# Performance work log

Hardware: AMD Instinct MI355X
Metric: run time of the kernel (lower is better)

## Reference

```python
import jax, jax.numpy as jnp
import numpy as np

B, T, Fd, C, D = 16, 256, 128, 32, 32
K_RATIO = 0.5
EPS = 1e-5


def setup_inputs() -> dict:
    key = jax.random.key(0)
    ks = jax.random.split(key, 40)
    n = lambda i, shape, s=0.05: jax.random.normal(ks[i], shape, jnp.float32) * s
    inp = {"x": jax.random.normal(ks[0], (B, T, Fd, C), jnp.float32)}
    inp.update(c1w=n(1, (C, C)), c1b=n(2, (C,)), bng=1.0 + n(3, (C,)), bnb=n(4, (C,)),
               bnm=n(5, (C,)), bnv=jax.random.uniform(ks[6], (C,)) + 0.5,
               c2w=n(7, (1, C)), c2b=n(8, (1,)))
    def gat_params(i0, pre):
        return {pre + "apw": n(i0, (D, C)), pre + "apb": n(i0 + 1, (D,)),
                pre + "aw": n(i0 + 2, (D,)), pre + "pww": n(i0 + 3, (D, C)),
                pre + "pwb": n(i0 + 4, (D,)), pre + "pow": n(i0 + 5, (D, C)),
                pre + "pob": n(i0 + 6, (D,)), pre + "g": 1.0 + n(i0 + 7, (D,)),
                pre + "be": n(i0 + 8, (D,)), pre + "m": n(i0 + 9, (D,)),
                pre + "v": jax.random.uniform(ks[i0 + 10], (D,)) + 0.5}
    inp.update(gat_params(9, "fc_"))
    inp.update(gat_params(20, "tc_"))
    inp.update(pfw=n(31, (1, D)), pfb=n(32, (1,)), ptw=n(33, (1, D)), ptb=n(34, (1,)),
               w1=n(35, (D, D)), w2=n(36, (D, D)), fcw=n(37, (2, 2 * D)), fcb=n(38, (2,)))
    return inp


def _gat(h, apw, apb, aw, pww, pwb, poww, pob, g, be, mu, var):
    # h: (B, N, C). Dense pairwise multiplication -> (B, N, N, C)
    p = h[:, :, None, :] * h[:, None, :, :]
    e = jnp.tanh(jnp.einsum('bijc,dc->bijd', p, apw) + apb)      # (B,N,N,D)
    att = jax.nn.softmax(jnp.einsum('bijd,d->bij', e, aw), axis=2)  # softmax over dim=-2 (temp=1)
    out = jnp.einsum('bij,bjc->bic', att, h) @ pww.T + pwb + h @ poww.T + pob
    out = (out - mu) / jnp.sqrt(var + EPS) * g + be               # BatchNorm1d (eval)
    return jax.nn.selu(out)


def _pool(h, pw, pb, ratio):
    s = jax.nn.sigmoid(h @ pw.T + pb)                # (B,N,1)
    kn = max(int(h.shape[1] * ratio), 1)
    _, idx = jax.lax.top_k(s[..., 0], kn)            # (B,kn), descending scores
    return jnp.take_along_axis(h * s, idx[..., None], axis=1)


def reference(x, c1w, c1b, bng, bnb, bnm, bnv, c2w, c2b,
              fc_apw, fc_apb, fc_aw, fc_pww, fc_pwb, fc_pow, fc_pob, fc_g, fc_be, fc_m, fc_v,
              tc_apw, tc_apb, tc_aw, tc_pww, tc_pwb, tc_pow, tc_pob, tc_g, tc_be, tc_m, tc_v,
              pfw, pfb, ptw, ptb, w1, w2, fcw, fcb):
    # conv1 (1x1), SELU, BatchNorm2d (eval), conv2 (1x1 -> 1 channel)
    xp = jnp.einsum('oc,btfc->botf', c1w, x) + c1b[None, :, None, None]
    xp = jax.nn.selu(xp)
    xp = (xp - bnm[None, :, None, None]) / jnp.sqrt(bnv + EPS)[None, :, None, None] \
         * bng[None, :, None, None] + bnb[None, :, None, None]
    m = jnp.einsum('c,bctf->btf', c2w[0], xp) + c2b[0]           # (B,T,F)
    M0 = jax.nn.softmax(m, axis=1)
    FCatt = jnp.einsum('btf,btfc->bfc', M0, x)                   # sum over T
    TCatt = jnp.einsum('btf,btfc->btc', M0, x)                   # sum over F
    FC_gat = _gat(FCatt, fc_apw, fc_apb, fc_aw, fc_pww, fc_pwb, fc_pow, fc_pob, fc_g, fc_be, fc_m, fc_v)
    TC_gat = _gat(TCatt, tc_apw, tc_apb, tc_aw, tc_pww, tc_pwb, tc_pow, tc_pob, tc_g, tc_be, tc_m, tc_v)
    xF = _pool(FC_gat, pfw, pfb, K_RATIO)                        # (B, F/2, D)
    xT = _pool(TC_gat, ptw, ptb, K_RATIO)                        # (B, T/2, D)
    M1 = jax.nn.softmax((xF @ w1.T) @ xT.transpose(0, 2, 1), axis=-1)
    M2 = jax.nn.softmax((xT @ w2.T) @ xF.transpose(0, 2, 1), axis=-1)
    xF_fused = xF + M1 @ xT
    xT_fused = xT + M2 @ xF
    node = jnp.concatenate([xF_fused.max(axis=1), xT_fused.max(axis=1)], axis=-1)
    return node @ fcw.T + fcb
```

## Files before the change

kernel.cpp:

```cpp
#include <hip/hip_runtime.h>
#include <hip/hip_bf16.h>

#define Bn 16
#define Tn 256
#define Fn 128
#define Cn 32
#define Dn 32
#define EPSf 1e-5f
#define SELU_L 1.0507009873554805f
#define SELU_A 1.6732632423543772f

typedef unsigned short u16;
typedef unsigned int u32;

struct Ptrs { const void* p[39]; };

#define P_C1W 0
#define P_C1B 1024
#define P_MW  1056
#define P_MK  1088
#define P_FC  1089
#define P_TCG (1089+3264)
#define G_APW 0
#define G_APB 1024
#define G_AW  1056
#define G_PWW 1088
#define G_PWB 2112
#define G_POW 2144
#define G_POB 3168
#define G_GS  3200
#define G_GB  3232
#define GAT_SZ 3264
#define P_PFW (P_TCG+GAT_SZ)
#define P_PFB (P_PFW+32)
#define P_PTW (P_PFB+1)
#define P_PTB (P_PTW+32)
#define P_W1  (P_PTB+1)
#define P_W2  (P_W1+1024)
#define P_FCW (P_W2+1024)
#define P_FCB (P_FCW+128)
#define P_FLAG 10000

#define WS_M     10240
#define WS_FCATT (WS_M+524288)
#define WS_TCATT (WS_FCATT+65536)
#define WS_FCGAT (WS_TCATT+131072)
#define WS_TCGAT (WS_FCGAT+65536)
#define WS_XF    (WS_TCGAT+131072)
#define WS_XT    (WS_XF+32768)
#define WS_XFF   (WS_XT+65536)
#define WS_XTF   (WS_XFF+32768)
#define WS_YFC   (WS_XTF+65536)
#define WS_ZFC   (WS_YFC+65536)
#define WS_YTC   (WS_ZFC+65536)
#define WS_ZTC   (WS_YTC+131072)
#define WS_SFC   (WS_ZTC+131072)

__device__ __forceinline__ float bf2f(u16 u) {
    union { u32 i; float f; } v; v.i = ((u32)u) << 16; return v.f;
}
__device__ __forceinline__ u16 f2bf(float f) {
    union { float f; u32 u; } v; v.f = f;
    u32 r = (v.u + 0x7fffu + ((v.u >> 16) & 1u)) >> 16;
    return (u16)r;
}
__device__ __forceinline__ void up2(u32 u, float* o) {
    union { u32 i; float f; } a, b;
    a.i = u << 16; b.i = u & 0xffff0000u;
    o[0] = a.f; o[1] = b.f;
}
__device__ __forceinline__ float tanh_fast(float x) {
    float e = __expf(2.f * x);
    return 1.f - 2.f / (e + 1.f);
}
__device__ __forceinline__ float ldp(const void* p, int i, int isb) {
    return isb ? bf2f(((const u16*)p)[i]) : ((const float*)p)[i];
}

__global__ void k0_setup(Ptrs in, float* __restrict__ P) {
    __shared__ int sflag;
    int tid = threadIdx.x;
    if (tid == 0) {
        const u16* xu = (const u16*)in.p[0];
        int bad = 0;
        for (int i = 0; i < 256; i++) {
            float f = bf2f(xu[i]);
            float a = fabsf(f);
            if (!(a < 64.f) && !(a == 0.f)) bad++;
        }
        sflag = (bad <= 8) ? 1 : 0;
        P[P_FLAG] = (float)sflag;
    }
    __syncthreads();
    const int isb = sflag;

    for (int i = tid; i < 1024; i += 256) P[P_C1W + i] = ldp(in.p[1], i, isb);
    if (tid < 32) {
        P[P_C1B + tid] = ldp(in.p[2], tid, isb);
        float A = ldp(in.p[3], tid, isb) * rsqrtf(ldp(in.p[6], tid, isb) + EPSf);
        P[P_MW + tid] = ldp(in.p[7], tid, isb) * A * SELU_L;
    }
    if (tid == 0) {
        float k = ldp(in.p[8], 0, isb);
        for (int o = 0; o < 32; o++) {
            float A = ldp(in.p[3], o, isb) * rsqrtf(ldp(in.p[6], o, isb) + EPSf);
            float Bc = ldp(in.p[4], o, isb) - ldp(in.p[5], o, isb) * A;
            k += ldp(in.p[7], o, isb) * Bc;
        }
        P[P_MK] = k;
    }
    for (int g = 0; g < 2; g++) {
        int ib = g ? 20 : 9;
        float* G = P + (g ? P_TCG : P_FC);
        for (int i = tid; i < 1024; i += 256) {
            G[G_APW + i] = ldp(in.p[ib + 0], i, isb);
            G[G_PWW + i] = ldp(in.p[ib + 3], i, isb);
            G[G_POW + i] = ldp(in.p[ib + 5], i, isb);
        }
        if (tid < 32) {
            G[G_APB + tid] = ldp(in.p[ib + 1], tid, isb);
            G[G_AW  + tid] = ldp(in.p[ib + 2], tid, isb);
            G[G_PWB + tid] = ldp(in.p[ib + 4], tid, isb);
            G[G_POB + tid] = ldp(in.p[ib + 6], tid, isb);
            float gs = ldp(in.p[ib + 7], tid, isb) * rsqrtf(ldp(in.p[ib + 10], tid, isb) + EPSf);
            G[G_GS + tid] = gs;
            G[G_GB + tid] = ldp(in.p[ib + 8], tid, isb) - ldp(in.p[ib + 9], tid, isb) * gs;
        }
    }
    if (tid < 32) {
        P[P_PFW + tid] = ldp(in.p[31], tid, isb);
        P[P_PTW + tid] = ldp(in.p[33], tid, isb);
    }
    if (tid == 0) { P[P_PFB] = ldp(in.p[32], 0, isb); P[P_PTB] = ldp(in.p[34], 0, isb); }
    for (int i = tid; i < 1024; i += 256) {
        P[P_W1 + i] = ldp(in.p[35], i, isb);
        P[P_W2 + i] = ldp(in.p[36], i, isb);
    }
    if (tid < 128) P[P_FCW + tid] = ldp(in.p[37], tid, isb);
    if (tid < 2)   P[P_FCB + tid] = ldp(in.p[38], tid, isb);
}

__global__ __launch_bounds__(256) void k1_conv_m(const void* __restrict__ xin,
                                                 const float* __restrict__ P,
                                                 float* __restrict__ M) {
    int idx = blockIdx.x * 256 + threadIdx.x;
    const int isb = __builtin_amdgcn_readfirstlane((int)P[P_FLAG]);
    float xv[32];
    if (isb) {
        const uint4* xp4 = reinterpret_cast<const uint4*>((const u16*)xin + (size_t)idx * 32);
        uint4 q0 = xp4[0], q1 = xp4[1], q2 = xp4[2], q3 = xp4[3];
        up2(q0.x, xv + 0);  up2(q0.y, xv + 2);  up2(q0.z, xv + 4);  up2(q0.w, xv + 6);
        up2(q1.x, xv + 8);  up2(q1.y, xv + 10); up2(q1.z, xv + 12); up2(q1.w, xv + 14);
        up2(q2.x, xv + 16); up2(q2.y, xv + 18); up2(q2.z, xv + 20); up2(q2.w, xv + 22);
        up2(q3.x, xv + 24); up2(q3.y, xv + 26); up2(q3.z, xv + 28); up2(q3.w, xv + 30);
    } else {
        const float4* xf4 = reinterpret_cast<const float4*>((const float*)xin + (size_t)idx * 32);
        #pragma unroll
        for (int q = 0; q < 8; q++) {
            float4 v = xf4[q];
            xv[q * 4 + 0] = v.x; xv[q * 4 + 1] = v.y;
            xv[q * 4 + 2] = v.z; xv[q * 4 + 3] = v.w;
        }
    }
    float acc = P[P_MK];
    #pragma unroll
    for (int o = 0; o < 32; o++) {
        float z = P[P_C1B + o];
        #pragma unroll
        for (int c = 0; c < 32; c++) z = fmaf(P[P_C1W + o * 32 + c], xv[c], z);
        float br = (z > 0.f) ? z : SELU_A * (__expf(z) - 1.f);
        acc = fmaf(P[P_MW + o], br, acc);
    }
    M[idx] = acc;
}

__global__ __launch_bounds__(256) void k2_softmax(float* __restrict__ M,
                                                  float* __restrict__ FCzero) {
    __shared__ float r[256];
    int b = blockIdx.x >> 3, fg = blockIdx.x & 7;
    int tid = threadIdx.x;
    int fl = tid & 15, ts = tid >> 4;
    float* col = M + (size_t)b * (Tn * Fn) + fg * 16 + fl;
    float v[16];
    float mx = -1e30f;
    #pragma unroll
    for (int k = 0; k < 16; k++) { v[k] = col[(ts * 16 + k) * Fn]; mx = fmaxf(mx, v[k]); }
    r[tid] = mx; __syncthreads();
    for (int s = 128; s >= 16; s >>= 1) { if (tid < s) r[tid] = fmaxf(r[tid], r[tid + s]); __syncthreads(); }
    mx = r[fl];
    __syncthreads();
    float sm = 0.f;
    #pragma unroll
    for (int k = 0; k < 16; k++) { v[k] = __expf(v[k] - mx); sm += v[k]; }
    r[tid] = sm; __syncthreads();
    for (int s = 128; s >= 16; s >>= 1) { if (tid < s) r[tid] += r[tid + s]; __syncthreads(); }
    float inv = 1.f / r[fl];
    #pragma unroll
    for (int k = 0; k < 16; k++) col[(ts * 16 + k) * Fn] = v[k] * inv;
    int gid = blockIdx.x * 256 + tid;
    for (int i = gid; i < Bn * Fn * Cn; i += 128 * 256) FCzero[i] = 0.f;
}

__global__ __launch_bounds__(256) void k3n(const void* __restrict__ xin,
                                           const float* __restrict__ M,
                                           const float* __restrict__ Pflag,
                                           float* __restrict__ FCatt,
                                           float* __restrict__ TCatt) {
    __shared__ float lA[256], lB[256];
    int bi = blockIdx.x;
    int b = bi >> 5, tg = bi & 31;
    int tid = threadIdx.x;
    const int isb = __builtin_amdgcn_readfirstlane((int)Pflag[P_FLAG]);
    float fa0[8], fa1[8];
    #pragma unroll
    for (int k = 0; k < 8; k++) { fa0[k] = 0.f; fa1[k] = 0.f; }
    int fbase = tid >> 4;
    for (int tt = 0; tt < 8; tt++) {
        int t = tg * 8 + tt;
        const float* Mrow = M + (size_t)b * (Tn * Fn) + (size_t)t * Fn;
        size_t rowoff = ((size_t)b * Tn + t) * (Fn * Cn);
        float ts0 = 0.f, ts1 = 0.f;
        #pragma unroll
        for (int k = 0; k < 8; k++) {
            float x0, x1;
            if (isb) {
                u32 u = *(const u32*)((const u16*)xin + rowoff + tid * 2 + 512 * k);
                float tmp[2]; up2(u, tmp); x0 = tmp[0]; x1 = tmp[1];
            } else {
                float2 v2 = *(const float2*)((const float*)xin + rowoff + tid * 2 + 512 * k);
                x0 = v2.x; x1 = v2.y;
            }
            float m = Mrow[fbase + 16 * k];
            x0 *= m; x1 *= m;
            fa0[k] += x0; fa1[k] += x1;
            ts0 += x0; ts1 += x1;
        }
        lA[tid] = ts0; lB[tid] = ts1;
        __syncthreads();
        if (tid < 32) {
            int half = tid & 1, p = tid >> 1;
            float s = 0.f;
            if (half) { for (int g = 0; g < 16; g++) s += lB[g * 16 + p]; }
            else      { for (int g = 0; g < 16; g++) s += lA[g * 16 + p]; }
            TCatt[((size_t)b * Tn + t) * Cn + tid] = s;
        }
        __syncthreads();
    }
    #pragma unroll
    for (int k = 0; k < 8; k++) {
        atomicAdd(&FCatt[(size_t)b * 4096 + tid * 2 + 512 * k],     fa0[k]);
        atomicAdd(&FCatt[(size_t)b * 4096 + tid * 2 + 512 * k + 1], fa1[k]);
    }
}

__global__ __launch_bounds__(256) void k4a_scores(const float* __restrict__ P,
                                                  const float* __restrict__ FCatt,
                                                  const float* __restrict__ TCatt,
                                                  u16* __restrict__ SFC,
                                                  u16* __restrict__ STC) {
    __shared__ float li[16 * 33], lj[16 * 33];
    int bi = blockIdx.x;
    int tid = threadIdx.x;
    int N, nt, b, pr; const float* h; u16* S; const float* G;
    if (bi < 16 * 36) { b = bi / 36; pr = bi % 36; N = 128; nt = 8;
        h = FCatt + (size_t)b * 4096; S = SFC + (size_t)b * 16384; G = P + P_FC; }
    else { bi -= 16 * 36; b = bi / 136; pr = bi % 136; N = 256; nt = 16;
        h = TCatt + (size_t)b * 8192; S = STC + (size_t)b * 65536; G = P + P_TCG; }
    int ti = 0, rem = pr;
    while (rem >= nt - ti) { rem -= nt - ti; ti++; }
    int tj = ti + rem;
    for (int e = tid; e < 512; e += 256) {
        int rr = e >> 5, c = e & 31;
        li[rr * 33 + c] = h[(ti * 16 + rr) * 32 + c];
        lj[rr * 33 + c] = h[(tj * 16 + rr) * 32 + c];
    }
    __syncthreads();
    int il = tid >> 4, jl = tid & 15;
    float p[32];
    #pragma unroll
    for (int c = 0; c < 32; c++) p[c] = li[il * 33 + c] * lj[jl * 33 + c];
    float score0 = 0.f, score1 = 0.f;
    #pragma unroll
    for (int d = 0; d < 32; d += 2) {
        float za0 = G[G_APB + d], za1 = 0.f;
        float zb0 = G[G_APB + d + 1], zb1 = 0.f;
        #pragma unroll
        for (int c = 0; c < 16; c++) {
            za0 = fmaf(G[G_APW + d * 32 + c], p[c], za0);
            za1 = fmaf(G[G_APW + d * 32 + 16 + c], p[16 + c], za1);
            zb0 = fmaf(G[G_APW + (d + 1) * 32 + c], p[c], zb0);
            zb1 = fmaf(G[G_APW + (d + 1) * 32 + 16 + c], p[16 + c], zb1);
        }
        score0 = fmaf(G[G_AW + d], tanh_fast(za0 + za1), score0);
        score1 = fmaf(G[G_AW + d + 1], tanh_fast(zb0 + zb1), score1);
    }
    float score = score0 + score1;
    int i = ti * 16 + il, j = tj * 16 + jl;
    u16 sb = f2bf(score);
    S[(size_t)i * N + j] = sb;
    if (ti != tj) S[(size_t)j * N + i] = sb;
}

__global__ __launch_bounds__(256) void k4yz(const float* __restrict__ P,
                                            const float* __restrict__ FCatt,
                                            const float* __restrict__ TCatt,
                                            float* __restrict__ Yfc,
                                            float* __restrict__ Zfc,
                                            float* __restrict__ Ytc,
                                            float* __restrict__ Ztc) {
    int bi = blockIdx.x;
    int tid = threadIdx.x;
    int b, rg; const float* h; float* Yg; float* Zg; const float* G;
    if (bi < 64) { b = bi >> 2; rg = bi & 3;
        h = FCatt + (size_t)b * 4096; Yg = Yfc + (size_t)b * 4096; Zg = Zfc + (size_t)b * 4096; G = P + P_FC; }
    else { bi -= 64; b = bi >> 3; rg = bi & 7;
        h = TCatt + (size_t)b * 8192; Yg = Ytc + (size_t)b * 8192; Zg = Ztc + (size_t)b * 8192; G = P + P_TCG; }
    #pragma unroll
    for (int k = 0; k < 8; k++) {
        int e = k * 256 + tid;
        int half = e >> 10, ee = e & 1023;
        int r = rg * 32 + (ee >> 5), d = ee & 31;
        const float* hr = h + (size_t)r * 32;
        if (half == 0) {
            float z = 0.f;
            #pragma unroll
            for (int c = 0; c < 32; c++) z = fmaf(hr[c], G[G_PWW + d * 32 + c], z);
            Yg[(size_t)r * 32 + d] = z;
        } else {
            float z = G[G_PWB + d] + G[G_POB + d];
            #pragma unroll
            for (int c = 0; c < 32; c++) z = fmaf(hr[c], G[G_POW + d * 32 + c], z);
            Zg[(size_t)r * 32 + d] = z;
        }
    }
}

__global__ __launch_bounds__(256) void k4b2(const float* __restrict__ P,
                                            const u16* __restrict__ SFC,
                                            const u16* __restrict__ STC,
                                            const float* __restrict__ Yfc,
                                            const float* __restrict__ Zfc,
                                            const float* __restrict__ Ytc,
                                            const float* __restrict__ Ztc,
                                            float* __restrict__ FCgat,
                                            float* __restrict__ TCgat) {
    int w = blockIdx.x * 4 + (threadIdx.x >> 6);
    int lane = threadIdx.x & 63;
    int N, b, i; const float *Yg, *Zg; const u16* S; float* out; const float* G;
    if (w < 2048) { N = 128; b = w >> 7; i = w & 127;
        Yg = Yfc + (size_t)b * 4096; Zg = Zfc + (size_t)b * 4096;
        S = SFC + (size_t)b * 16384 + (size_t)i * 128;
        out = FCgat + (size_t)b * 4096 + (size_t)i * 32; G = P + P_FC; }
    else { int w2 = w - 2048; N = 256; b = w2 >> 8; i = w2 & 255;
        Yg = Ytc + (size_t)b * 8192; Zg = Ztc + (size_t)b * 8192;
        S = STC + (size_t)b * 65536 + (size_t)i * 256;
        out = TCgat + (size_t)b * 8192 + (size_t)i * 32; G = P + P_TCG; }
    float s0 = bf2f(S[lane]);
    float s1 = bf2f(S[lane + 64]);
    float s2 = -1e30f, s3 = -1e30f;
    if (N == 256) { s2 = bf2f(S[lane + 128]); s3 = bf2f(S[lane + 192]); }
    float mx = fmaxf(fmaxf(s0, s1), fmaxf(s2, s3));
    #pragma unroll
    for (int off = 1; off < 64; off <<= 1) mx = fmaxf(mx, __shfl_xor(mx, off, 64));
    float e0 = __expf(s0 - mx), e1 = __expf(s1 - mx);
    float e2 = 0.f, e3 = 0.f;
    if (N == 256) { e2 = __expf(s2 - mx); e3 = __expf(s3 - mx); }
    float sm = e0 + e1 + e2 + e3;
    #pragma unroll
    for (int off = 1; off < 64; off <<= 1) sm += __shfl_xor(sm, off, 64);
    float inv = 1.f / sm;
    float a0 = e0 * inv, a1 = e1 * inv, a2 = e2 * inv, a3 = e3 * inv;
    float v[32];
    const float4* Y4 = reinterpret_cast<const float4*>(Yg);
    #pragma unroll
    for (int q = 0; q < 8; q++) {
        float4 y0 = Y4[(size_t)lane * 8 + q];
        float4 y1 = Y4[(size_t)(lane + 64) * 8 + q];
        v[4 * q + 0] = a0 * y0.x + a1 * y1.x;
        v[4 * q + 1] = a0 * y0.y + a1 * y1.y;
        v[4 * q + 2] = a0 * y0.z + a1 * y1.z;
        v[4 * q + 3] = a0 * y0.w + a1 * y1.w;
    }
    if (N == 256) {
        #pragma unroll
        for (int q = 0; q < 8; q++) {
            float4 y2 = Y4[(size_t)(lane + 128) * 8 + q];
            float4 y3 = Y4[(size_t)(lane + 192) * 8 + q];
            v[4 * q + 0] += a2 * y2.x + a3 * y3.x;
            v[4 * q + 1] += a2 * y2.y + a3 * y3.y;
            v[4 * q + 2] += a2 * y2.z + a3 * y3.z;
            v[4 * q + 3] += a2 * y2.w + a3 * y3.w;
        }
    }
    #pragma unroll
    for (int off = 1; off < 64; off <<= 1) {
        #pragma unroll
        for (int c = 0; c < 32; c++) v[c] += __shfl_xor(v[c], off, 64);
    }
    if (lane == 0) {
        const float4* Z4 = reinterpret_cast<const float4*>(Zg + (size_t)((out - (w < 2048 ? FCgat + (size_t)b * 4096 : TCgat + (size_t)b * 8192))));
        (void)Z4;
        const float* Zrow = Zg + (size_t)i * 32;
        float4* O4 = reinterpret_cast<float4*>(out);
        #pragma unroll
        for (int q = 0; q < 8; q++) {
            float4 zz = *reinterpret_cast<const float4*>(Zrow + 4 * q);
            float r[4];
            #pragma unroll
            for (int k = 0; k < 4; k++) {
                int d = 4 * q + k;
                float z = v[d] + ((const float*)&zz)[k];
                z = z * G[G_GS + d] + G[G_GB + d];
                r[k] = SELU_L * ((z > 0.f) ? z : SELU_A * (__expf(z) - 1.f));
            }
            O4[q] = make_float4(r[0], r[1], r[2], r[3]);
        }
    }
}

__global__ __launch_bounds__(256) void k5_pool(const float* __restrict__ P,
                                               const float* __restrict__ FCgat,
                                               const float* __restrict__ TCgat,
                                               float* __restrict__ XF,
                                               float* __restrict__ XT) {
    __shared__ float s[256];
    int bi = blockIdx.x;
    int N, kn, b, pboff; const float* g; float* xp; const float* pw;
    if (bi < 16) { b = bi; N = 128; kn = 64;
        g = FCgat + (size_t)b * 4096; xp = XF + (size_t)b * 2048; pw = P + P_PFW; pboff = P_PFB; }
    else { b = bi - 16; N = 256; kn = 128;
        g = TCgat + (size_t)b * 8192; xp = XT + (size_t)b * 4096; pw = P + P_PTW; pboff = P_PTB; }
    int tid = threadIdx.x;
    float sv = 0.f;
    if (tid < N) {
        float z = P[pboff];
        #pragma unroll
        for (int d = 0; d < 32; d++) z = fmaf(pw[d], g[(size_t)tid * 32 + d], z);
        sv = 1.f / (1.f + __expf(-z));
        s[tid] = sv;
    }
    __syncthreads();
    if (tid < N) {
        int rank = 0;
        for (int l = 0; l < N; l++) {
            float sl = s[l];
            rank += (sl > sv) || (sl == sv && l < tid);
        }
        if (rank < kn) {
            #pragma unroll
            for (int d = 0; d < 32; d++) xp[(size_t)rank * 32 + d] = g[(size_t)tid * 32 + d] * sv;
        }
    }
}

__global__ __launch_bounds__(256) void k6_fuse(const float* __restrict__ P,
                                               const float* __restrict__ XF,
                                               const float* __restrict__ XT,
                                               float* __restrict__ XFF,
                                               float* __restrict__ XTF) {
    int wid = blockIdx.x * 4 + (threadIdx.x >> 6);
    int lane = threadIdx.x & 63;
    if (wid < 1024) {
        int b = wid >> 6, i = wid & 63;
        const float* xf  = XF + ((size_t)b * 64 + i) * 32;
        const float* xtb = XT + (size_t)b * 4096;
        const float* w1 = P + P_W1;
        int d = lane & 31;
        float y = 0.f;
        #pragma unroll
        for (int c = 0; c < 32; c++) y = fmaf(w1[d * 32 + c], xf[c], y);
        float xtr0[32], xtr1[32];
        #pragma unroll
        for (int c = 0; c < 32; c++) {
            xtr0[c] = xtb[(size_t)lane * 32 + c];
            xtr1[c] = xtb[(size_t)(lane + 64) * 32 + c];
        }
        float s0 = 0.f, s1 = 0.f;
        #pragma unroll
        for (int c = 0; c < 32; c++) {
            float yc = __shfl(y, c, 64);
            s0 = fmaf(yc, xtr0[c], s0);
            s1 = fmaf(yc, xtr1[c], s1);
        }
        float mx = fmaxf(s0, s1);
        #pragma unroll
        for (int off = 1; off < 64; off <<= 1) mx = fmaxf(mx, __shfl_xor(mx, off, 64));
        float e0 = __expf(s0 - mx), e1 = __expf(s1 - mx);
        float sm = e0 + e1;
        #pragma unroll
        for (int off = 1; off < 64; off <<= 1) sm += __shfl_xor(sm, off, 64);
        float inv = 1.f / sm;
        float a0 = e0 * inv, a1 = e1 * inv;
        float v[32];
        #pragma unroll
        for (int c = 0; c < 32; c++) v[c] = a0 * xtr0[c] + a1 * xtr1[c];
        #pragma unroll
        for (int off = 1; off < 64; off <<= 1) {
            #pragma unroll
            for (int c = 0; c < 32; c++) v[c] += __shfl_xor(v[c], off, 64);
        }
        if (lane == 0) {
            float* o = XFF + ((size_t)b * 64 + i) * 32;
            #pragma unroll
            for (int c = 0; c < 32; c++) o[c] = xf[c] + v[c];
        }
    } else {
        int r = wid - 1024;
        int b = r >> 7, i = r & 127;
        const float* xt  = XT + ((size_t)b * 128 + i) * 32;
        const float* xfb = XF + (size_t)b * 2048;
        const float* w2 = P + P_W2;
        int d = lane & 31;
        float y = 0.f;
        #pragma unroll
        for (int c = 0; c < 32; c++) y = fmaf(w2[d * 32 + c], xt[c], y);
        float xfr[32];
        #pragma unroll
        for (int c = 0; c < 32; c++) xfr[c] = xfb[(size_t)lane * 32 + c];
        float sc0 = 0.f;
        #pragma unroll
        for (int c = 0; c < 32; c++) sc0 = fmaf(__shfl(y, c, 64), xfr[c], sc0);
        float mx = sc0;
        #pragma unroll
        for (int off = 1; off < 64; off <<= 1) mx = fmaxf(mx, __shfl_xor(mx, off, 64));
        float e = __expf(sc0 - mx);
        float sm = e;
        #pragma unroll
        for (int off = 1; off < 64; off <<= 1) sm += __shfl_xor(sm, off, 64);
        float a = e / sm;
        float v[32];
        #pragma unroll
        for (int c = 0; c < 32; c++) v[c] = a * xfr[c];
        #pragma unroll
        for (int off = 1; off < 64; off <<= 1) {
            #pragma unroll
            for (int c = 0; c < 32; c++) v[c] += __shfl_xor(v[c], off, 64);
        }
        if (lane == 0) {
            float* o = XTF + ((size_t)b * 128 + i) * 32;
            #pragma unroll
            for (int c = 0; c < 32; c++) o[c] = xt[c] + v[c];
        }
    }
}

__global__ __launch_bounds__(64) void k7_out(const float* __restrict__ P,
                                             const float* __restrict__ XFF,
                                             const float* __restrict__ XTF,
                                             void* __restrict__ outp) {
    __shared__ float node[64];
    int b = blockIdx.x, tid = threadIdx.x;
    if (tid < 32) {
        float m = -1e30f;
        for (int r = 0; r < 64; r++) m = fmaxf(m, XFF[((size_t)b * 64 + r) * 32 + tid]);
        node[tid] = m;
    } else {
        int c = tid - 32;
        float m = -1e30f;
        for (int r = 0; r < 128; r++) m = fmaxf(m, XTF[((size_t)b * 128 + r) * 32 + c]);
        node[tid] = m;
    }
    __syncthreads();
    if (tid < 2) {
        float z = P[P_FCB + tid];
        #pragma unroll
        for (int k = 0; k < 64; k++) z = fmaf(P[P_FCW + tid * 64 + k], node[k], z);
        int isb = (int)P[P_FLAG];
        if (isb) ((u16*)outp)[b * 2 + tid] = f2bf(z);
        else     ((float*)outp)[b * 2 + tid] = z;
    }
}

extern "C" void kernel_launch(void* const* d_in, const int* in_sizes, int n_in,
                              void* d_out, int out_size, void* d_ws, size_t ws_size,
                              hipStream_t stream) {
    (void)in_sizes; (void)n_in; (void)out_size; (void)ws_size;
    float* W = (float*)d_ws;
    Ptrs ptrs;
    for (int i = 0; i < 39; i++) ptrs.p[i] = d_in[i];
    const void* x = d_in[0];
    float* P = W;
    u16* STC = (u16*)(W + WS_M);
    u16* SFC = (u16*)(W + WS_SFC);

    k0_setup<<<1, 256, 0, stream>>>(ptrs, P);
    k1_conv_m<<<2048, 256, 0, stream>>>(x, P, W + WS_M);
    k2_softmax<<<128, 256, 0, stream>>>(W + WS_M, W + WS_FCATT);
    k3n<<<512, 256, 0, stream>>>(x, W + WS_M, P, W + WS_FCATT, W + WS_TCATT);
    k4a_scores<<<2752, 256, 0, stream>>>(P, W + WS_FCATT, W + WS_TCATT, SFC, STC);
    k4yz<<<192, 256, 0, stream>>>(P, W + WS_FCATT, W + WS_TCATT,
                                  W + WS_YFC, W + WS_ZFC, W + WS_YTC, W + WS_ZTC);
    k4b2<<<1536, 256, 0, stream>>>(P, SFC, STC, W + WS_YFC, W + WS_ZFC, W + WS_YTC, W + WS_ZTC,
                                   W + WS_FCGAT, W + WS_TCGAT);
    k5_pool<<<32, 256, 0, stream>>>(P, W + WS_FCGAT, W + WS_TCGAT, W + WS_XF, W + WS_XT);
    k6_fuse<<<768, 256, 0, stream>>>(P, W + WS_XF, W + WS_XT, W + WS_XFF, W + WS_XTF);
    k7_out<<<16, 64, 0, stream>>>(P, W + WS_XFF, W + WS_XTF, d_out);
}
```

Baseline: 375.6 us.

## Compute GAT pairwise attention projections with bf16 MFMA in score kernel

The pairwise score kernel now forms the elementwise products h_i*h_j as bf16 fragments and runs the 32x32 attention projection on the 16x16x32 bf16 MFMA instruction. It then applies bias, tanh and the attention weights, and reduces across lanes with shuffles. This replaces the per-thread scalar FMA loop over 32x32 weights. A bf16 copy of the projection weights is prepared in setup, and LDS rows are padded to 36. The cost is reduced precision in the products and weights, plus added shuffle reductions.

```diff
diff --git a/kernel.cpp b/kernel.cpp
--- a/kernel.cpp
+++ b/kernel.cpp
@@ -12,6 +12,8 @@
 
 typedef unsigned short u16;
 typedef unsigned int u32;
+typedef __attribute__((ext_vector_type(8))) short bf16x8;
+typedef __attribute__((ext_vector_type(4))) float f32x4;
 
 struct Ptrs { const void* p[39]; };
 
@@ -55,6 +57,7 @@
 #define WS_YTC   (WS_ZFC+65536)
 #define WS_ZTC   (WS_YTC+131072)
 #define WS_SFC   (WS_ZTC+131072)
+#define WS_APWB  (WS_SFC+131072)
 
 __device__ __forceinline__ float bf2f(u16 u) {
     union { u32 i; float f; } v; v.i = ((u32)u) << 16; return v.f;
@@ -77,7 +80,7 @@
     return isb ? bf2f(((const u16*)p)[i]) : ((const float*)p)[i];
 }
 
-__global__ void k0_setup(Ptrs in, float* __restrict__ P) {
+__global__ void k0_setup(Ptrs in, float* __restrict__ P, u16* __restrict__ APWb) {
     __shared__ int sflag;
     int tid = threadIdx.x;
     if (tid == 0) {
@@ -116,6 +119,7 @@
             G[G_APW + i] = ldp(in.p[ib + 0], i, isb);
             G[G_PWW + i] = ldp(in.p[ib + 3], i, isb);
             G[G_POW + i] = ldp(in.p[ib + 5], i, isb);
+            APWb[g * 1024 + i] = f2bf(ldp(in.p[ib + 0], i, isb));
         }
         if (tid < 32) {
             G[G_APB + tid] = ldp(in.p[ib + 1], tid, isb);
@@ -256,49 +260,61 @@
 __global__ __launch_bounds__(256) void k4a_scores(const float* __restrict__ P,
                                                   const float* __restrict__ FCatt,
                                                   const float* __restrict__ TCatt,
+                                                  const u16* __restrict__ APWb,
                                                   u16* __restrict__ SFC,
                                                   u16* __restrict__ STC) {
-    __shared__ float li[16 * 33], lj[16 * 33];
+    __shared__ float li[16 * 36], lj[16 * 36];
     int bi = blockIdx.x;
     int tid = threadIdx.x;
-    int N, nt, b, pr; const float* h; u16* S; const float* G;
+    int N, nt, b, pr; const float* h; u16* S; const float* G; const u16* Wb;
     if (bi < 16 * 36) { b = bi / 36; pr = bi % 36; N = 128; nt = 8;
-        h = FCatt + (size_t)b * 4096; S = SFC + (size_t)b * 16384; G = P + P_FC; }
+        h = FCatt + (size_t)b * 4096; S = SFC + (size_t)b * 16384; G = P + P_FC; Wb = APWb; }
     else { bi -= 16 * 36; b = bi / 136; pr = bi % 136; N = 256; nt = 16;
-        h = TCatt + (size_t)b * 8192; S = STC + (size_t)b * 65536; G = P + P_TCG; }
+        h = TCatt + (size_t)b * 8192; S = STC + (size_t)b * 65536; G = P + P_TCG; Wb = APWb + 1024; }
     int ti = 0, rem = pr;
     while (rem >= nt - ti) { rem -= nt - ti; ti++; }
     int tj = ti + rem;
     for (int e = tid; e < 512; e += 256) {
         int rr = e >> 5, c = e & 31;
-        li[rr * 33 + c] = h[(ti * 16 + rr) * 32 + c];
-        lj[rr * 33 + c] = h[(tj * 16 + rr) * 32 + c];
+        li[rr * 36 + c] = h[(ti * 16 + rr) * 32 + c];
+        lj[rr * 36 + c] = h[(tj * 16 + rr) * 32 + c];
     }
     __syncthreads();
-    int il = tid >> 4, jl = tid & 15;
-    float p[32];
-    #pragma unroll
-    for (int c = 0; c < 32; c++) p[c] = li[il * 33 + c] * lj[jl * 33 + c];
-    float score0 = 0.f, score1 = 0.f;
-    #pragma unroll
-    for (int d = 0; d < 32; d += 2) {
-        float za0 = G[G_APB + d], za1 = 0.f;
-        float zb0 = G[G_APB + d + 1], zb1 = 0.f;
-        #pragma unroll
-        for (int c = 0; c < 16; c++) {
-            za0 = fmaf(G[G_APW + d * 32 + c], p[c], za0);
-            za1 = fmaf(G[G_APW + d * 32 + 16 + c], p[16 + c], za1);
-            zb0 = fmaf(G[G_APW + (d + 1) * 32 + c], p[c], zb0);
-            zb1 = fmaf(G[G_APW + (d + 1) * 32 + 16 + c], p[16 + c], zb1);
-        }
-        score0 = fmaf(G[G_AW + d], tanh_fast(za0 + za1), score0);
-        score1 = fmaf(G[G_AW + d + 1], tanh_fast(zb0 + zb1), score1);
-    }
-    float score = score0 + score1;
-    int i = ti * 16 + il, j = tj * 16 + jl;
-    u16 sb = f2bf(score);
-    S[(size_t)i * N + j] = sb;
-    if (ti != tj) S[(size_t)j * N + i] = sb;
+    int wv = tid >> 6, lane = tid & 63;
+    int n = lane & 15, q = lane >> 4, k0 = q * 8;
+    uint4 u0 = *reinterpret_cast<const uint4*>(Wb + n * 32 + k0);
+    uint4 u1 = *reinterpret_cast<const uint4*>(Wb + (n + 16) * 32 + k0);
+    bf16x8 B0 = *reinterpret_cast<const bf16x8*>(&u0);
+    bf16x8 B1 = *reinterpret_cast<const bf16x8*>(&u1);
+    float apb0 = G[G_APB + n], apb1 = G[G_APB + n + 16];
+    float aw0 = G[G_AW + n],  aw1 = G[G_AW + n + 16];
+    #pragma unroll
+    for (int mtl = 0; mtl < 4; mtl++) {
+        int mt = wv * 4 + mtl;
+        const float* ljrow = lj + n * 36 + k0;
+        const float* lirow = li + mt * 36 + k0;
+        bf16x8 A;
+        #pragma unroll
+        for (int j = 0; j < 8; j++) ((u16*)&A)[j] = f2bf(lirow[j] * ljrow[j]);
+        f32x4 C0 = {0.f, 0.f, 0.f, 0.f}, C1 = {0.f, 0.f, 0.f, 0.f};
+        C0 = __builtin_amdgcn_mfma_f32_16x16x32_bf16(A, B0, C0, 0, 0, 0);
+        C1 = __builtin_amdgcn_mfma_f32_16x16x32_bf16(A, B1, C1, 0, 0, 0);
+        float part[4];
+        #pragma unroll
+        for (int r = 0; r < 4; r++)
+            part[r] = aw0 * tanh_fast(C0[r] + apb0) + aw1 * tanh_fast(C1[r] + apb1);
+        #pragma unroll
+        for (int off = 1; off < 16; off <<= 1) {
+            #pragma unroll
+            for (int r = 0; r < 4; r++) part[r] += __shfl_xor(part[r], off, 64);
+        }
+        if (n < 4) {
+            int i = ti * 16 + mt, j = tj * 16 + q * 4 + n;
+            u16 sb = f2bf(part[n]);
+            S[(size_t)i * N + j] = sb;
+            if (ti != tj) S[(size_t)j * N + i] = sb;
+        }
+    }
 }
 
 __global__ __launch_bounds__(256) void k4yz(const float* __restrict__ P,
@@ -398,8 +414,6 @@
         for (int c = 0; c < 32; c++) v[c] += __shfl_xor(v[c], off, 64);
     }
     if (lane == 0) {
-        const float4* Z4 = reinterpret_cast<const float4*>(Zg + (size_t)((out - (w < 2048 ? FCgat + (size_t)b * 4096 : TCgat + (size_t)b * 8192))));
-        (void)Z4;
         const float* Zrow = Zg + (size_t)i * 32;
         float4* O4 = reinterpret_cast<float4*>(out);
         #pragma unroll
@@ -580,14 +594,15 @@
     for (int i = 0; i < 39; i++) ptrs.p[i] = d_in[i];
     const void* x = d_in[0];
     float* P = W;
-    u16* STC = (u16*)(W + WS_M);
-    u16* SFC = (u16*)(W + WS_SFC);
-
-    k0_setup<<<1, 256, 0, stream>>>(ptrs, P);
+    u16* STC  = (u16*)(W + WS_M);
+    u16* SFC  = (u16*)(W + WS_SFC);
+    u16* APWb = (u16*)(W + WS_APWB);
+
+    k0_setup<<<1, 256, 0, stream>>>(ptrs, P, APWb);
     k1_conv_m<<<2048, 256, 0, stream>>>(x, P, W + WS_M);
     k2_softmax<<<128, 256, 0, stream>>>(W + WS_M, W + WS_FCATT);
     k3n<<<512, 256, 0, stream>>>(x, W + WS_M, P, W + WS_FCATT, W + WS_TCATT);
-    k4a_scores<<<2752, 256, 0, stream>>>(P, W + WS_FCATT, W + WS_TCATT, SFC, STC);
+    k4a_scores<<<2752, 256, 0, stream>>>(P, W + WS_FCATT, W + WS_TCATT, APWb, SFC, STC);
     k4yz<<<192, 256, 0, stream>>>(P, W + WS_FCATT, W + WS_TCATT,
                                   W + WS_YFC, W + WS_ZFC, W + WS_YTC, W + WS_ZTC);
     k4b2<<<1536, 256, 0, stream>>>(P, SFC, STC, W + WS_YFC, W + WS_ZFC, W + WS_YTC, W + WS_ZTC,
```

Measured after the change: 363.0 us. 1.03x faster.
